# Performance work log

Measured on AMD Instinct MI355X. Metric: run time of the kernel, lower is better.

The kernel has to match this reference:

```python
import jax, jax.numpy as jnp
import numpy as np

EPS = 1e-5
CLIP = 1.0

@jax.custom_vjp
def ste_sign(x):
    return jnp.sign(x)

def _ste_fwd(x):
    return jnp.sign(x), x

def _ste_bwd(x, g):
    return (g * (jnp.abs(x) <= CLIP).astype(g.dtype),)

ste_sign.defvjp(_ste_fwd, _ste_bwd)

def conv2d(x, w, stride, pad):
    return jax.lax.conv_general_dilated(
        x, w, window_strides=(stride, stride), padding=[(pad, pad), (pad, pad)],
        dimension_numbers=('NCHW', 'OIHW', 'NCHW'))

def bn(x, g, b, m, v):
    inv = g / jnp.sqrt(v + EPS)
    return x * inv[None, :, None, None] + (b - m * inv)[None, :, None, None]

def setup_inputs() -> dict:
    key = jax.random.key(0)
    ks = jax.random.split(key, 16)
    def rn(k, shape, scale=0.05):
        return jax.random.normal(k, shape, dtype=jnp.float32) * scale
    C = [64, 128, 128, 192, 192]
    d = {}
    d['x'] = jax.random.normal(ks[0], (128, 1, 128, 128), dtype=jnp.float32)
    d['conv1_w'] = rn(ks[1], (C[0], 1, 3, 3), 0.3)
    d['conv1_b'] = rn(ks[2], (C[0],))
    d['w2'] = rn(ks[3], (C[1], C[0], 3, 3), 0.3)
    d['w3'] = rn(ks[4], (C[2], C[1], 3, 3), 0.3)
    d['w4'] = rn(ks[5], (C[3], C[2], 3, 3), 0.3)
    d['w5'] = rn(ks[6], (C[4], C[3], 1, 1), 0.3)
    d['conv6_w'] = rn(ks[7], (12, C[4], 1, 1), 0.1)
    d['conv6_b'] = rn(ks[8], (12,))
    d['fc_w'] = rn(ks[9], (12, 12), 0.2)
    d['fc_b'] = rn(ks[10], (12,))
    for i, c in enumerate(C):
        kk = jax.random.split(jax.random.fold_in(key, 100 + i), 4)
        d[f'bn{i+1}_g'] = 1.0 + rn(kk[0], (c,), 0.1)
        d[f'bn{i+1}_b'] = rn(kk[1], (c,), 0.1)
        d[f'bn{i+1}_m'] = rn(kk[2], (c,), 0.1)
        d[f'bn{i+1}_v'] = 1.0 + jnp.abs(rn(kk[3], (c,), 0.1))
    return d

def reference(x, conv1_w, conv1_b, w2, w3, w4, w5, conv6_w, conv6_b, fc_w, fc_b,
              bn1_g, bn1_b, bn1_m, bn1_v, bn2_g, bn2_b, bn2_m, bn2_v,
              bn3_g, bn3_b, bn3_m, bn3_v, bn4_g, bn4_b, bn4_m, bn4_v,
              bn5_g, bn5_b, bn5_m, bn5_v):
    # conv1 (float) + BN + ReLU
    h = conv2d(x, conv1_w, 2, 1) + conv1_b[None, :, None, None]
    h = jax.nn.relu(bn(h, bn1_g, bn1_b, bn1_m, bn1_v))
    # binarized conv blocks: sign(activation) conv sign(weight)
    h = conv2d(ste_sign(h), ste_sign(w2), 1, 1)
    h = jax.nn.relu(bn(h, bn2_g, bn2_b, bn2_m, bn2_v))
    h = conv2d(ste_sign(h), ste_sign(w3), 2, 1)
    h = jax.nn.relu(bn(h, bn3_g, bn3_b, bn3_m, bn3_v))
    h = conv2d(ste_sign(h), ste_sign(w4), 1, 1)
    h = jax.nn.relu(bn(h, bn4_g, bn4_b, bn4_m, bn4_v))
    h = conv2d(ste_sign(h), ste_sign(w5), 1, 0)
    h = jax.nn.relu(bn(h, bn5_g, bn5_b, bn5_m, bn5_v))
    # 1x1 conv to classes, global average pool, FC, softmax
    h = conv2d(h, conv6_w, 1, 0) + conv6_b[None, :, None, None]
    h = jnp.mean(h, axis=(2, 3))  # [B, num_classes]
    logits = h @ fc_w.T + fc_b
    return jax.nn.softmax(logits, axis=1)
```

## Files before the change

kernel.cpp:

```cpp
#include <hip/hip_runtime.h>
#include <cstdint>

using u64 = unsigned long long;
using u32 = unsigned int;
typedef __attribute__((ext_vector_type(4))) int int4v;

struct PrepArgs {
  const float* bng[5]; const float* bnb[5]; const float* bnm[5]; const float* bnv[5];
  float* inv1; float* cc1; float* inv5; float* cc5;
  int* thr[3]; int* flp[3];
  const float* w[4];
  u64* wp[4]; u64* wz[4];
  u32* flags;
};

__global__ __launch_bounds__(256) void prep_all(PrepArgs a) {
  int i = blockIdx.x * 256 + threadIdx.x;
  if (i < 704) {
    const int off[6] = {0, 64, 192, 320, 512, 704};
    int l = 0;
    while (i >= off[l + 1]) ++l;
    int c = i - off[l];
    float iv = __fdiv_rn(a.bng[l][c], __fsqrt_rn(__fadd_rn(a.bnv[l][c], 1e-5f)));
    float cb = __fsub_rn(a.bnb[l][c], __fmul_rn(a.bnm[l][c], iv));
    if (l == 0) { a.inv1[c] = iv; a.cc1[c] = cb; }
    else if (l == 4) { a.inv5[c] = iv; a.cc5[c] = cb; }
    else {
      auto pred = [&](int v_) {
        return __fadd_rn(__fmul_rn((float)v_, iv), cb) > 0.f;
      };
      int Tx, fl;
      if (iv == 0.f) { Tx = pred(0) ? -100000 : 100000; fl = 0; }
      else if (iv > 0.f) {
        if (pred(-2048)) { Tx = -100000; fl = 0; }
        else if (!pred(2048)) { Tx = 100000; fl = 0; }
        else {
          int lo = -2048, hi = 2048;
          while (hi - lo > 1) { int md = (lo + hi) >> 1; if (pred(md)) hi = md; else lo = md; }
          Tx = hi; fl = 0;
        }
      } else {
        if (pred(2048)) { Tx = -100000; fl = -1; }
        else if (!pred(-2048)) { Tx = 100000; fl = -1; }
        else {
          int lo = -2048, hi = 2048;
          while (hi - lo > 1) { int md = (lo + hi) >> 1; if (pred(md)) lo = md; else hi = md; }
          Tx = lo ^ -1; fl = -1;
        }
      }
      a.thr[l - 1][c] = Tx; a.flp[l - 1][c] = fl;
    }
    return;
  }
  int j = i - 704;
  if (j >= 7488) return;
  const int poff[5] = {0, 1152, 3456, 6912, 7488};
  const int ICt[4] = {64, 128, 128, 192};
  const int Kt[4]  = {9, 9, 9, 1};
  const int Wt[4]  = {1, 2, 2, 3};
  int l = 0;
  while (j >= poff[l + 1]) ++l;
  int idx = j - poff[l];
  int W = Wt[l], K = Kt[l], IC = ICt[l];
  int wi = idx % W;
  int rest = idx / W;
  int t = rest % K;
  int oc = rest / K;
  u64 p = 0, z = 0;
  int icbase = wi * 64;
  int nb = IC - icbase; if (nb > 64) nb = 64;
  const float* w = a.w[l];
  for (int b = 0; b < nb; ++b) {
    float f = w[((size_t)oc * IC + (icbase + b)) * K + t];
    if (f > 0.f) p |= (1ull << b);
    else if (f == 0.f) z |= (1ull << b);
  }
  a.wp[l][idx] = p;
  a.wz[l][idx] = z;
  if (z) atomicOr(a.flags + l, 1u);
}

template <int CINW, int COUT>
__global__ __launch_bounds__(256) void prep_bfrag(const float* __restrict__ w,
                                                  signed char* __restrict__ bf) {
  constexpr int NKC = 9 * CINW;
  constexpr int NT = COUT / 16;
  constexpr int CIN = 64 * CINW;
  int idx = blockIdx.x * 256 + threadIdx.x;
  if (idx >= NT * NKC * 64) return;
  int lane = idx & 63;
  int rest = idx >> 6;
  int kc = rest % NKC;
  int t = rest / NKC;
  int tap = kc / CINW, wd = kc % CINW;
  int n = t * 16 + (lane & 15);
  int icb = wd * 64 + (lane >> 4) * 16;
  signed char* dst = bf + (size_t)idx * 16;
#pragma unroll
  for (int i = 0; i < 16; ++i) {
    float f = w[((size_t)n * CIN + icb + i) * 9 + tap];
    dst[i] = (f > 0.f) ? 1 : ((f < 0.f) ? -1 : 0);
  }
}

__global__ __launch_bounds__(256) void pad_x(const float* __restrict__ x,
                                             float* __restrict__ xpad) {
  int idx = blockIdx.x * 256 + threadIdx.x;
  int c = idx & 127, r = (idx >> 7) & 127, n = idx >> 14;
  xpad[((size_t)n * 130 + r + 1) * 136 + c + 1] = x[idx];
}

__global__ __launch_bounds__(256) void conv1_bin(
    const float* __restrict__ xpad, const float* __restrict__ w1, const float* __restrict__ b1,
    const float* __restrict__ inv1, const float* __restrict__ cc1,
    u64* __restrict__ a1p) {
  int tid = threadIdx.x, lane = tid & 63;
  int rb = __builtin_amdgcn_readfirstlane(tid >> 6);
  int blk = blockIdx.x;
  int y = (blk % 16) * 4 + rb;
  int n = blk / 16;
  float W[9];
#pragma unroll
  for (int t = 0; t < 9; ++t) W[t] = w1[lane * 9 + t];
  float bias = b1[lane], iv = inv1[lane], cb = cc1[lane];
  const float* sb = xpad + ((size_t)n * 130 + 2 * y) * 136;
  float A[12], B[12], C[12];
  u64 rowm = 0;
  int xb = 0;

#define FLD(BUF, POFF)                                     \
  _Pragma("unroll") for (int _r = 0; _r < 3; ++_r)         \
  _Pragma("unroll") for (int _j = 0; _j < 4; ++_j)         \
    BUF[_r * 4 + _j] = sb[_r * 136 + (POFF) + _j];
#define FPX(XO, B0F, C0, B1F, C1, B2F, C2) {                          \
  float acc = 0.f;                                                    \
  _Pragma("unroll") for (int _r = 0; _r < 3; ++_r)                    \
    acc += B0F[_r * 4 + (C0)] * W[_r * 3 + 0]                         \
         + B1F[_r * 4 + (C1)] * W[_r * 3 + 1]                         \
         + B2F[_r * 4 + (C2)] * W[_r * 3 + 2];                        \
  float h = __fadd_rn(acc, bias);                                     \
  float bnv = __fadd_rn(__fmul_rn(h, iv), cb);                        \
  u64 _m = __ballot(bnv > 0.f);                                       \
  rowm = (lane == (XO)) ? _m : rowm; }
#define FSTEP(BA, BB, BC, POFF, XB)  \
  FLD(BC, (POFF) + 8);               \
  FPX((XB), BA, 0, BA, 1, BA, 2);    \
  FPX((XB) + 1, BA, 2, BA, 3, BB, 0);

  FLD(A, 0); FLD(B, 4);
  for (int g = 0; g < 10; ++g) {
    FSTEP(A, B, C, 0, xb);
    FSTEP(B, C, A, 4, xb + 2);
    FSTEP(C, A, B, 8, xb + 4);
    sb += 12; xb += 6;
  }
  FSTEP(A, B, C, 0, xb);
  FSTEP(B, C, A, 4, xb + 2);
  a1p[((size_t)n * 66 + (y + 1)) * 68 + lane + 1] = rowm;
#undef FLD
#undef FPX
#undef FSTEP
}

template <int CINW, int COUT, int STRIDE, int IN_HW, int OUT_HW, int MT, int NSPLIT, int OPAD>
__global__ __launch_bounds__(256) void bconv_mfma(
    const u64* __restrict__ ain, const signed char* __restrict__ bf,
    const int* __restrict__ thr, const int* __restrict__ flp,
    u64* __restrict__ aout) {
  constexpr int IPW = IN_HW + 4;
  constexpr int NKC = 9 * CINW;
  constexpr int NT = COUT / 16;
  constexpr int NTW = NT / NSPLIT;
  constexpr int OCW = (COUT + 63) / 64;
  constexpr int XG = OUT_HW / (16 * MT);
  constexpr int FRAG = NTW * NKC * 64;
  constexpr int CPT = FRAG / 256;
  constexpr int NW32 = NTW / 2;
  __shared__ int4v bs[FRAG];

  int tid = threadIdx.x, lane = tid & 63;
  int wv = __builtin_amdgcn_readfirstlane(tid >> 6);
  int b = blockIdx.x;
  int split = b % NSPLIT;
  int pos = (b / NSPLIT) * 4 + wv;
  int xg = pos % XG;
  int rest = pos / XG;
  int y = rest % OUT_HW;
  int n = rest / OUT_HW;
  int t0 = split * NTW;
  int m = lane & 15;
  int kg = lane >> 4;

  const int4v* bfv = (const int4v*)bf;

  int4v breg[CPT];
  const int4v* bsrc = bfv + (size_t)t0 * NKC * 64;
#pragma unroll
  for (int i = 0; i < CPT; ++i) breg[i] = bsrc[tid + i * 256];

  int4v af[MT * NKC];
#pragma unroll
  for (int mt = 0; mt < MT; ++mt) {
    int x = (xg * MT + mt) * 16 + m;
    const u64* abase = ain + (((size_t)n * (IN_HW + 2) + STRIDE * y) * IPW
                              + (size_t)STRIDE * x) * CINW;
#pragma unroll
    for (int dy = 0; dy < 3; ++dy)
#pragma unroll
      for (int dx = 0; dx < 3; ++dx)
#pragma unroll
        for (int wd = 0; wd < CINW; ++wd) {
          u64 aw = abase[((size_t)dy * IPW + dx) * CINW + wd];
          u32 t16 = (u32)(aw >> (kg * 16)) & 0xFFFFu;
          int4v v;
          v.x = (int)((((t16      ) & 0xFu) * 0x00204081u) & 0x01010101u);
          v.y = (int)((((t16 >> 4 ) & 0xFu) * 0x00204081u) & 0x01010101u);
          v.z = (int)((((t16 >> 8 ) & 0xFu) * 0x00204081u) & 0x01010101u);
          v.w = (int)((((t16 >> 12) & 0xFu) * 0x00204081u) & 0x01010101u);
          af[mt * NKC + (dy * 3 + dx) * CINW + wd] = v;
        }
  }

#pragma unroll
  for (int i = 0; i < CPT; ++i) bs[tid + i * 256] = breg[i];
  __syncthreads();

  u32 acc32[MT][NW32];
#pragma unroll
  for (int mt = 0; mt < MT; ++mt)
#pragma unroll
    for (int wl = 0; wl < NW32; ++wl) acc32[mt][wl] = 0;

#pragma unroll
  for (int tl = 0; tl < NTW; ++tl) {
    int t = t0 + tl;
    int4v c[MT];
#pragma unroll
    for (int mt = 0; mt < MT; ++mt) c[mt] = (int4v){0, 0, 0, 0};
#pragma unroll
    for (int kc = 0; kc < NKC; ++kc) {
      int4v bb = bs[(tl * NKC + kc) * 64 + lane];
#pragma unroll
      for (int mt = 0; mt < MT; ++mt)
        c[mt] = __builtin_amdgcn_mfma_i32_16x16x64_i8(af[mt * NKC + kc], bb, c[mt], 0, 0, 0);
    }
    int tx = thr[t * 16 + m];
    int fl = flp[t * 16 + m];
#pragma unroll
    for (int mt = 0; mt < MT; ++mt) {
      u64 b0 = __ballot((c[mt].x ^ fl) >= tx);
      u64 b1 = __ballot((c[mt].y ^ fl) >= tx);
      u64 b2 = __ballot((c[mt].z ^ fl) >= tx);
      u64 b3 = __ballot((c[mt].w ^ fl) >= tx);
      u64 s01 = (m & 1) ? b1 : b0;
      u64 s23 = (m & 1) ? b3 : b2;
      u64 bsel = (m & 2) ? s23 : s01;
      u32 slice = (u32)(bsel >> ((m >> 2) * 16)) & 0xFFFFu;
      acc32[mt][tl >> 1] |= slice << ((tl & 1) * 16);
    }
  }

  if (kg == 0) {
    u32* out32 = (u32*)aout;
#pragma unroll
    for (int mt = 0; mt < MT; ++mt) {
      int x = (xg * MT + mt) * 16 + m;
      size_t px32;
      if (OPAD)
        px32 = (((size_t)n * (OUT_HW + 2) + (y + 1)) * (OUT_HW + 4) + (x + 1)) * (OCW * 2);
      else
        px32 = (((size_t)n * OUT_HW + y) * OUT_HW + x) * (OCW * 2);
#pragma unroll
      for (int wl = 0; wl < NW32; ++wl)
        out32[px32 + (t0 >> 1) + wl] = acc32[mt][wl];
    }
  }
}

#define NCH5 8
__global__ __launch_bounds__(192) void bconv5_pool(
    const u64* __restrict__ ain, const u64* __restrict__ wp, const u64* __restrict__ wz,
    const u32* __restrict__ flag, const float* __restrict__ inv5, const float* __restrict__ cc5,
    float* __restrict__ partial) {
  int n = blockIdx.x / NCH5, ch = blockIdx.x % NCH5;
  int oc = threadIdx.x;
  u64 W0 = wp[oc * 3], W1 = wp[oc * 3 + 1], W2 = wp[oc * 3 + 2];
  bool anyz = (*flag != 0u);
  float iv = inv5[oc], cb = cc5[oc];
  const u64* sb = ain + ((size_t)n * 1024 + ch * 128) * 3;
  u64 A0, A1, A2, B0, B1, B2, C0, C1, C2;
  float acc = 0.f;
#define LD5(P, a0_, a1_, a2_) { a0_ = sb[(P) * 3]; a1_ = sb[(P) * 3 + 1]; a2_ = sb[(P) * 3 + 2]; }
#define PX5(a0_, a1_, a2_) {                                                   \
  int _pa = __popcll(a0_) + __popcll(a1_) + __popcll(a2_);                     \
  int _s = __popcll(a0_ & W0) + __popcll(a1_ & W1) + __popcll(a2_ & W2);       \
  int _val = 2 * _s - _pa;                                                     \
  if (anyz) _val += __popcll(a0_ & wz[oc * 3]) + __popcll(a1_ & wz[oc * 3 + 1])\
                  + __popcll(a2_ & wz[oc * 3 + 2]);                            \
  float _b = __fadd_rn(__fmul_rn((float)_val, iv), cb);                        \
  acc += fmaxf(_b, 0.f); }
  LD5(0, A0, A1, A2); LD5(1, B0, B1, B2);
  for (int g = 0; g < 42; ++g) {
    LD5(2, C0, C1, C2); PX5(A0, A1, A2);
    LD5(3, A0, A1, A2); PX5(B0, B1, B2);
    LD5(4, B0, B1, B2); PX5(C0, C1, C2);
    sb += 9;
  }
  PX5(A0, A1, A2); PX5(B0, B1, B2);
  partial[((size_t)n * NCH5 + ch) * 192 + oc] = acc;
#undef LD5
#undef PX5
}

__global__ __launch_bounds__(192) void head2(
    const float* __restrict__ partial,
    const float* __restrict__ w6, const float* __restrict__ b6,
    const float* __restrict__ fw, const float* __restrict__ fb,
    float* __restrict__ out) {
  __shared__ float pool_s[192];
  __shared__ float h6s[12];
  __shared__ float lgs[12];
  int n = blockIdx.x, t = threadIdx.x;
  float s = 0.f;
#pragma unroll
  for (int ch = 0; ch < NCH5; ++ch) s += partial[((size_t)n * NCH5 + ch) * 192 + t];
  pool_s[t] = s;
  __syncthreads();
  if (t < 12) {
    float a = 0.f;
    for (int c = 0; c < 192; ++c) a += pool_s[c] * w6[t * 192 + c];
    h6s[t] = b6[t] + a * (1.0f / 1024.0f);
  }
  __syncthreads();
  if (t < 12) {
    float s2 = fb[t];
    for (int k = 0; k < 12; ++k) s2 += h6s[k] * fw[t * 12 + k];
    lgs[t] = s2;
  }
  __syncthreads();
  if (t == 0) {
    float mx = -1e30f;
    for (int j = 0; j < 12; ++j) mx = fmaxf(mx, lgs[j]);
    float e[12], se = 0.f;
    for (int j = 0; j < 12; ++j) { e[j] = expf(lgs[j] - mx); se += e[j]; }
    for (int j = 0; j < 12; ++j) out[n * 12 + j] = e[j] / se;
  }
}

extern "C" void kernel_launch(void* const* d_in, const int* in_sizes, int n_in,
                              void* d_out, int out_size, void* d_ws, size_t ws_size,
                              hipStream_t stream) {
  const float* x   = (const float*)d_in[0];
  const float* w1  = (const float*)d_in[1];
  const float* b1  = (const float*)d_in[2];
  const float* w2  = (const float*)d_in[3];
  const float* w3  = (const float*)d_in[4];
  const float* w4  = (const float*)d_in[5];
  const float* w5  = (const float*)d_in[6];
  const float* w6  = (const float*)d_in[7];
  const float* b6  = (const float*)d_in[8];
  const float* fcw = (const float*)d_in[9];
  const float* fcb = (const float*)d_in[10];
  float* out = (float*)d_out;

  char* ws = (char*)d_ws;
  size_t off = 0;
  auto alloc = [&](size_t bytes) -> void* {
    void* p = ws + off;
    off += (bytes + 255) & ~(size_t)255;
    return p;
  };
  size_t xp_sz = (size_t)128 * 130 * 136 * 4;
  size_t a1_sz = (size_t)128 * 66 * 68 * 1 * 8;
  size_t a2_sz = (size_t)128 * 66 * 68 * 2 * 8;
  size_t a3_sz = (size_t)128 * 34 * 36 * 2 * 8;
  float* xpad = (float*)alloc(xp_sz);
  u64* a1p = (u64*)alloc(a1_sz);
  u64* a2p = (u64*)alloc(a2_sz);
  u64* a3p = (u64*)alloc(a3_sz);
  size_t zero_sz = xp_sz + a1_sz + a2_sz + a3_sz;
  u64* a4p = (u64*)alloc((size_t)128 * 32 * 32 * 3 * 8);
  float* partial = (float*)alloc((size_t)128 * NCH5 * 192 * 4);
  float* inv1 = (float*)alloc(64 * 4);
  float* cc1  = (float*)alloc(64 * 4);
  float* inv5 = (float*)alloc(192 * 4);
  float* cc5  = (float*)alloc(192 * 4);
  int* thr2 = (int*)alloc(128 * 4); int* flp2 = (int*)alloc(128 * 4);
  int* thr3 = (int*)alloc(128 * 4); int* flp3 = (int*)alloc(128 * 4);
  int* thr4 = (int*)alloc(192 * 4); int* flp4 = (int*)alloc(192 * 4);
  u64* wp2 = (u64*)alloc(128 * 9 * 1 * 8);
  u64* wz2 = (u64*)alloc(128 * 9 * 1 * 8);
  u64* wp3 = (u64*)alloc(128 * 9 * 2 * 8);
  u64* wz3 = (u64*)alloc(128 * 9 * 2 * 8);
  u64* wp4 = (u64*)alloc(192 * 9 * 2 * 8);
  u64* wz4 = (u64*)alloc(192 * 9 * 2 * 8);
  u64* wp5 = (u64*)alloc(192 * 1 * 3 * 8);
  u64* wz5 = (u64*)alloc(192 * 1 * 3 * 8);
  u32* flags = (u32*)alloc(4 * sizeof(u32));
  signed char* bf2 = (signed char*)alloc((size_t)8 * 9 * 64 * 16);
  signed char* bf3 = (signed char*)alloc((size_t)8 * 18 * 64 * 16);
  signed char* bf4 = (signed char*)alloc((size_t)12 * 18 * 64 * 16);
  (void)ws_size; (void)n_in; (void)in_sizes; (void)out_size;

  hipMemsetAsync(xpad, 0, zero_sz, stream);
  hipMemsetAsync(flags, 0, 4 * sizeof(u32), stream);

  PrepArgs pa;
  for (int l = 0; l < 5; ++l) {
    pa.bng[l] = (const float*)d_in[11 + 4 * l + 0];
    pa.bnb[l] = (const float*)d_in[11 + 4 * l + 1];
    pa.bnm[l] = (const float*)d_in[11 + 4 * l + 2];
    pa.bnv[l] = (const float*)d_in[11 + 4 * l + 3];
  }
  pa.inv1 = inv1; pa.cc1 = cc1; pa.inv5 = inv5; pa.cc5 = cc5;
  pa.thr[0] = thr2; pa.flp[0] = flp2;
  pa.thr[1] = thr3; pa.flp[1] = flp3;
  pa.thr[2] = thr4; pa.flp[2] = flp4;
  pa.w[0] = w2; pa.w[1] = w3; pa.w[2] = w4; pa.w[3] = w5;
  pa.wp[0] = wp2; pa.wp[1] = wp3; pa.wp[2] = wp4; pa.wp[3] = wp5;
  pa.wz[0] = wz2; pa.wz[1] = wz3; pa.wz[2] = wz4; pa.wz[3] = wz5;
  pa.flags = flags;
  prep_all<<<32, 256, 0, stream>>>(pa);

  prep_bfrag<1, 128><<<(8 * 9 * 64 + 255) / 256, 256, 0, stream>>>(w2, bf2);
  prep_bfrag<2, 128><<<(8 * 18 * 64 + 255) / 256, 256, 0, stream>>>(w3, bf3);
  prep_bfrag<2, 192><<<(12 * 18 * 64 + 255) / 256, 256, 0, stream>>>(w4, bf4);

  pad_x<<<(128 * 128 * 128) / 256, 256, 0, stream>>>(x, xpad);

  conv1_bin<<<128 * 16, 256, 0, stream>>>(xpad, w1, b1, inv1, cc1, a1p);

  bconv_mfma<1, 128, 1, 64, 64, 2, 2, 1><<<8192, 256, 0, stream>>>(
      a1p, bf2, thr2, flp2, a2p);

  bconv_mfma<2, 128, 2, 64, 32, 1, 4, 1><<<8192, 256, 0, stream>>>(
      a2p, bf3, thr3, flp3, a3p);

  bconv_mfma<2, 192, 1, 32, 32, 1, 6, 0><<<12288, 256, 0, stream>>>(
      a3p, bf4, thr4, flp4, a4p);

  bconv5_pool<<<128 * NCH5, 192, 0, stream>>>(a4p, wp5, wz5, flags + 3, inv5, cc5, partial);

  head2<<<128, 192, 0, stream>>>(partial, w6, b6, fcw, fcb, out);
}
```

Measured before the change: 224.2 us.

## Compute all output-channel tiles per wave with staged, register-prefetched weight fragments

Each block now covers every output-channel tile instead of splitting channels across blocks. Weight fragments are streamed through shared memory in stages, and the next stage is prefetched into registers while the current one feeds the MFMAs. This removes the repeated activation gather and unpacking that happened in every channel-split block, and it cuts the grid size. The cost is serial work per wave, an extra pair of barriers per stage, and fewer blocks to keep the device occupied.

```diff
diff --git a/kernel.cpp b/kernel.cpp
--- a/kernel.cpp
+++ b/kernel.cpp
@@ -162,7 +162,7 @@
 #undef FSTEP
 }
 
-template <int CINW, int COUT, int STRIDE, int IN_HW, int OUT_HW, int MT, int NSPLIT, int OPAD>
+template <int CINW, int COUT, int STRIDE, int IN_HW, int OUT_HW, int MT, int TSTG, int OPAD>
 __global__ __launch_bounds__(256) void bconv_mfma(
     const u64* __restrict__ ain, const signed char* __restrict__ bf,
     const int* __restrict__ thr, const int* __restrict__ flp,
@@ -170,33 +170,32 @@
   constexpr int IPW = IN_HW + 4;
   constexpr int NKC = 9 * CINW;
   constexpr int NT = COUT / 16;
-  constexpr int NTW = NT / NSPLIT;
+  constexpr int NSTG = NT / TSTG;
   constexpr int OCW = (COUT + 63) / 64;
   constexpr int XG = OUT_HW / (16 * MT);
-  constexpr int FRAG = NTW * NKC * 64;
-  constexpr int CPT = FRAG / 256;
-  constexpr int NW32 = NTW / 2;
+  constexpr int FRAG = TSTG * NKC * 64;
+  constexpr int CPT = (FRAG + 255) / 256;
+  constexpr int NW32 = NT / 2;
   __shared__ int4v bs[FRAG];
 
   int tid = threadIdx.x, lane = tid & 63;
   int wv = __builtin_amdgcn_readfirstlane(tid >> 6);
-  int b = blockIdx.x;
-  int split = b % NSPLIT;
-  int pos = (b / NSPLIT) * 4 + wv;
+  int pos = blockIdx.x * 4 + wv;
   int xg = pos % XG;
   int rest = pos / XG;
   int y = rest % OUT_HW;
   int n = rest / OUT_HW;
-  int t0 = split * NTW;
   int m = lane & 15;
   int kg = lane >> 4;
 
   const int4v* bfv = (const int4v*)bf;
 
   int4v breg[CPT];
-  const int4v* bsrc = bfv + (size_t)t0 * NKC * 64;
-#pragma unroll
-  for (int i = 0; i < CPT; ++i) breg[i] = bsrc[tid + i * 256];
+#pragma unroll
+  for (int i = 0; i < CPT; ++i) {
+    int ix = tid + i * 256;
+    if (FRAG % 256 == 0 || ix < FRAG) breg[i] = bfv[ix];
+  }
 
   int4v af[MT * NKC];
 #pragma unroll
@@ -221,10 +220,6 @@
         }
   }
 
-#pragma unroll
-  for (int i = 0; i < CPT; ++i) bs[tid + i * 256] = breg[i];
-  __syncthreads();
-
   u32 acc32[MT][NW32];
 #pragma unroll
   for (int mt = 0; mt < MT; ++mt)
@@ -232,31 +227,50 @@
     for (int wl = 0; wl < NW32; ++wl) acc32[mt][wl] = 0;
 
 #pragma unroll
-  for (int tl = 0; tl < NTW; ++tl) {
-    int t = t0 + tl;
-    int4v c[MT];
-#pragma unroll
-    for (int mt = 0; mt < MT; ++mt) c[mt] = (int4v){0, 0, 0, 0};
-#pragma unroll
-    for (int kc = 0; kc < NKC; ++kc) {
-      int4v bb = bs[(tl * NKC + kc) * 64 + lane];
-#pragma unroll
-      for (int mt = 0; mt < MT; ++mt)
-        c[mt] = __builtin_amdgcn_mfma_i32_16x16x64_i8(af[mt * NKC + kc], bb, c[mt], 0, 0, 0);
+  for (int s = 0; s < NSTG; ++s) {
+    __syncthreads();
+#pragma unroll
+    for (int i = 0; i < CPT; ++i) {
+      int ix = tid + i * 256;
+      if (FRAG % 256 == 0 || ix < FRAG) bs[ix] = breg[i];
     }
-    int tx = thr[t * 16 + m];
-    int fl = flp[t * 16 + m];
-#pragma unroll
-    for (int mt = 0; mt < MT; ++mt) {
-      u64 b0 = __ballot((c[mt].x ^ fl) >= tx);
-      u64 b1 = __ballot((c[mt].y ^ fl) >= tx);
-      u64 b2 = __ballot((c[mt].z ^ fl) >= tx);
-      u64 b3 = __ballot((c[mt].w ^ fl) >= tx);
-      u64 s01 = (m & 1) ? b1 : b0;
-      u64 s23 = (m & 1) ? b3 : b2;
-      u64 bsel = (m & 2) ? s23 : s01;
-      u32 slice = (u32)(bsel >> ((m >> 2) * 16)) & 0xFFFFu;
-      acc32[mt][tl >> 1] |= slice << ((tl & 1) * 16);
+    __syncthreads();
+    if (s + 1 < NSTG) {
+      const int4v* src = bfv + (size_t)(s + 1) * FRAG;
+#pragma unroll
+      for (int i = 0; i < CPT; ++i) {
+        int ix = tid + i * 256;
+        if (FRAG % 256 == 0 || ix < FRAG) breg[i] = src[ix];
+      }
+    }
+#pragma unroll
+    for (int tl = 0; tl < TSTG; ++tl) {
+      constexpr int dummy = 0; (void)dummy;
+      int4v c[MT];
+#pragma unroll
+      for (int mt = 0; mt < MT; ++mt) c[mt] = (int4v){0, 0, 0, 0};
+#pragma unroll
+      for (int kc = 0; kc < NKC; ++kc) {
+        int4v bb = bs[(tl * NKC + kc) * 64 + lane];
+#pragma unroll
+        for (int mt = 0; mt < MT; ++mt)
+          c[mt] = __builtin_amdgcn_mfma_i32_16x16x64_i8(af[mt * NKC + kc], bb, c[mt], 0, 0, 0);
+      }
+      const int t = s * TSTG + tl;
+      int tx = thr[t * 16 + m];
+      int fl = flp[t * 16 + m];
+#pragma unroll
+      for (int mt = 0; mt < MT; ++mt) {
+        u64 b0 = __ballot((c[mt].x ^ fl) >= tx);
+        u64 b1 = __ballot((c[mt].y ^ fl) >= tx);
+        u64 b2 = __ballot((c[mt].z ^ fl) >= tx);
+        u64 b3 = __ballot((c[mt].w ^ fl) >= tx);
+        u64 s01 = (m & 1) ? b1 : b0;
+        u64 s23 = (m & 1) ? b3 : b2;
+        u64 bsel = (m & 2) ? s23 : s01;
+        u32 slice = (u32)(bsel >> ((m >> 2) * 16)) & 0xFFFFu;
+        acc32[mt][t >> 1] |= slice << ((t & 1) * 16);
+      }
     }
   }
 
@@ -272,7 +286,7 @@
         px32 = (((size_t)n * OUT_HW + y) * OUT_HW + x) * (OCW * 2);
 #pragma unroll
       for (int wl = 0; wl < NW32; ++wl)
-        out32[px32 + (t0 >> 1) + wl] = acc32[mt][wl];
+        out32[px32 + wl] = acc32[mt][wl];
     }
   }
 }
@@ -430,13 +444,13 @@
 
   conv1_bin<<<128 * 16, 256, 0, stream>>>(xpad, w1, b1, inv1, cc1, a1p);
 
-  bconv_mfma<1, 128, 1, 64, 64, 2, 2, 1><<<8192, 256, 0, stream>>>(
+  bconv_mfma<1, 128, 1, 64, 64, 2, 2, 1><<<4096, 256, 0, stream>>>(
       a1p, bf2, thr2, flp2, a2p);
 
-  bconv_mfma<2, 128, 2, 64, 32, 1, 4, 1><<<8192, 256, 0, stream>>>(
+  bconv_mfma<2, 128, 2, 64, 32, 1, 1, 1><<<2048, 256, 0, stream>>>(
       a2p, bf3, thr3, flp3, a3p);
 
-  bconv_mfma<2, 192, 1, 32, 32, 1, 6, 0><<<12288, 256, 0, stream>>>(
+  bconv_mfma<2, 192, 1, 32, 32, 1, 1, 0><<<2048, 256, 0, stream>>>(
       a3p, bf4, thr4, flp4, a4p);
 
   bconv5_pool<<<128 * NCH5, 192, 0, stream>>>(a4p, wp5, wz5, flags + 3, inv5, cc5, partial);
```

After: 224.0 us. About the same (-0.1%).
